# Kernel tuning notes

Hardware: AMD Instinct MI355X
Metric: run time of the kernel (lower is better)

## Reference

```python
import jax, jax.numpy as jnp
import numpy as np

N = 100_000   # nodes
E = 800_000   # edges
D = 128       # hidden_dim
L = 4         # layer_num
G = 512       # graphs in batch
T = 10        # target_dim
BN_EPS = 1e-5


def setup_inputs() -> dict:
    key = jax.random.key(0)
    ks = jax.random.split(key, 16)
    return {
        "x": jax.random.randint(ks[0], (N, 9), 0, 64),
        "edge_index": jax.random.randint(ks[1], (2, E), 0, N),
        "batch": jnp.sort(jax.random.randint(ks[2], (N,), 0, G)),
        "edge_attr": jax.random.randint(ks[3], (E, 3), 0, 8),
        "atom_emb": jax.random.normal(ks[4], (9, 64, D), jnp.float32) * 0.1,
        "W": jax.random.normal(ks[5], (L, D, D), jnp.float32) * 0.05,
        "b": jax.random.normal(ks[6], (L, D), jnp.float32) * 0.01,
        "root": jax.random.normal(ks[7], (L, D), jnp.float32) * 0.1,
        "bond_emb": jax.random.normal(ks[8], (L, 3, 8, D), jnp.float32) * 0.1,
        "gamma": jnp.ones((L, D), jnp.float32),
        "beta": jnp.zeros((L, D), jnp.float32),
        "W1": jax.random.normal(ks[9], (D, D), jnp.float32) * 0.05,
        "b1": jax.random.normal(ks[10], (D,), jnp.float32) * 0.01,
        "W2": jax.random.normal(ks[11], (D, T), jnp.float32) * 0.05,
        "b2": jax.random.normal(ks[12], (T,), jnp.float32) * 0.01,
    }


def reference(x, edge_index, batch, edge_attr, atom_emb, W, b, root,
              bond_emb, gamma, beta, W1, b1, W2, b2):
    # AtomEncoder: sum of 9 per-feature embeddings -> [N, D]
    h = atom_emb[jnp.arange(9)[None, :], x].sum(axis=1)

    row, col = edge_index[0], edge_index[1]  # source j, target i
    # degree(row, N) + 1 (same every layer)
    deg = jax.ops.segment_sum(jnp.ones((E,), h.dtype), row, num_segments=N) + 1.0
    dinv = deg ** -0.5
    norm = dinv[row] * dinv[col]  # [E]

    feat3 = jnp.arange(3)[None, :]
    for l in range(L):
        hl = h @ W[l] + b[l]                                   # linear
        e = bond_emb[l][feat3, edge_attr].sum(axis=1)          # BondEncoder [E, D]
        msg = norm[:, None] * jax.nn.relu(hl[row] + e)         # gather + message
        aggr = jax.ops.segment_sum(msg, col, num_segments=N)   # scatter-add
        h = aggr + jax.nn.relu(hl + root[l]) / deg[:, None]
        if l < L - 1:
            mu = h.mean(axis=0)
            var = jnp.var(h, axis=0)                           # biased, as torch BN train
            h = (h - mu) / jnp.sqrt(var + BN_EPS) * gamma[l] + beta[l]
            h = jax.nn.relu(h)
        # dropout is identity in eval mode

    # global mean pool over graphs
    counts = jax.ops.segment_sum(jnp.ones((N,), h.dtype), batch, num_segments=G)
    hg = jax.ops.segment_sum(h, batch, num_segments=G) / jnp.maximum(counts, 1.0)[:, None]

    # output MLP: ReLU -> Linear -> ReLU -> Linear
    hh = jax.nn.relu(hg)
    hh = jax.nn.relu(hh @ W1 + b1)
    return hh @ W2 + b2
```

## Files before the change

### kernel.cpp

```cpp
#include <hip/hip_runtime.h>
#include <hip/hip_fp16.h>

#define NN 100000
#define NE 800000
#define DD 128
#define NL 4
#define NG 512
#define NT 10
#define BN_EPS 1e-5f
#define SCAN_B 1024
#define CHUNK 7

typedef __attribute__((ext_vector_type(4))) float f32x4;
typedef __attribute__((ext_vector_type(8))) _Float16 f16x8;

__device__ __forceinline__ float atomAddF(float* p, float v) {
  return unsafeAtomicAdd(p, v);
}


__global__ __launch_bounds__(256) void edge_count_kernel(
    const int* __restrict__ ei, int* __restrict__ degcnt,
    int* __restrict__ incnt, int* __restrict__ erank) {
  int t = blockIdx.x * 256 + threadIdx.x;
  if (t * 4 >= NE) return;
  int4 s = *reinterpret_cast<const int4*>(&ei[t * 4]);
  int4 d = *reinterpret_cast<const int4*>(&ei[NE + t * 4]);
  atomicAdd(&degcnt[s.x], 1);
  atomicAdd(&degcnt[s.y], 1);
  atomicAdd(&degcnt[s.z], 1);
  atomicAdd(&degcnt[s.w], 1);
  int4 r;
  r.x = atomicAdd(&incnt[d.x], 1);
  r.y = atomicAdd(&incnt[d.y], 1);
  r.z = atomicAdd(&incnt[d.z], 1);
  r.w = atomicAdd(&incnt[d.w], 1);
  *reinterpret_cast<int4*>(&erank[t * 4]) = r;
}


__global__ __launch_bounds__(256) void tables_kernel(
    const float* __restrict__ W, __half* __restrict__ Wf,
    const float* __restrict__ atom_emb, __half* __restrict__ aemb16,
    const int* __restrict__ batch, int* __restrict__ gstart) {
  const int idx = blockIdx.x * 256 + threadIdx.x;
  if (idx < NL * 8 * 4 * 64) {
    int lane = idx & 63;
    int c = (idx >> 6) & 3;
    int t = (idx >> 8) & 7;
    int l = idx >> 11;
    const float* Wl = W + l * DD * DD;
    __half* o = Wf + idx * 8;
    int n = t * 16 + (lane & 15);
    int k0 = c * 32 + (lane >> 4) * 8;
#pragma unroll
    for (int i = 0; i < 8; ++i) o[i] = (__half)Wl[(k0 + i) * DD + n];
  }
  if (idx < 9 * 64 * 32) {
    float4 v = *reinterpret_cast<const float4*>(&atom_emb[idx * 4]);
    union { __half2 hh[2]; int2 i2; } u;
    u.hh[0] = __floats2half2_rn(v.x, v.y);
    u.hh[1] = __floats2half2_rn(v.z, v.w);
    *reinterpret_cast<int2*>(&aemb16[idx * 4]) = u.i2;
  }
  if (idx <= NG) {
    if (idx == NG) {
      gstart[NG] = NN;
    } else {
      int lo = 0, hi = NN;
      while (lo < hi) {
        int m = (lo + hi) >> 1;
        if (batch[m] < idx) lo = m + 1; else hi = m;
      }
      gstart[idx] = lo;
    }
  }
}


__global__ __launch_bounds__(256) void atom_encoder_kernel(
    const int* __restrict__ x, const __half* __restrict__ aemb16,
    __half* __restrict__ h) {
  __shared__ int xs[16 * 9];
  const int nb = blockIdx.x * 16;
  const int t = threadIdx.x;
  if (t < 144) {
    int gi = nb * 9 + t;
    xs[t] = (gi < NN * 9) ? x[gi] : 0;
  }
  __syncthreads();
  const int n = nb + (t >> 4);
  const int q8 = t & 15;
  if (n >= NN) return;
  const f16x8* av = reinterpret_cast<const f16x8*>(aemb16);
  float acc[8] = {};
#pragma unroll
  for (int f = 0; f < 9; ++f) {
    int r = xs[(t >> 4) * 9 + f];
    f16x8 v = av[(f * 64 + r) * 16 + q8];
#pragma unroll
    for (int i = 0; i < 8; ++i) acc[i] += (float)v[i];
  }
  union { __half2 hh[4]; int4 i4; } u;
#pragma unroll
  for (int i = 0; i < 4; ++i)
    u.hh[i] = __floats2half2_rn(acc[2 * i], acc[2 * i + 1]);
  *reinterpret_cast<int4*>(&h[n * DD + q8 * 8]) = u.i4;
}


__global__ __launch_bounds__(256) void scan1_kernel(
    const int* __restrict__ in, int* __restrict__ out, int* __restrict__ bsum,
    const int* __restrict__ degcnt, float* __restrict__ degrecip,
    float* __restrict__ dinv, int n) {
  __shared__ int s[256];
  int base = blockIdx.x * SCAN_B + threadIdx.x * 4;
  int v[4] = {0, 0, 0, 0};
  if (base + 3 < n) {
    int4 t = *reinterpret_cast<const int4*>(&in[base]);
    v[0] = t.x; v[1] = t.y; v[2] = t.z; v[3] = t.w;
  } else {
    for (int i = 0; i < 4; ++i) v[i] = (base + i < n) ? in[base + i] : 0;
  }
  for (int i = 0; i < 4; ++i) {
    if (base + i < n) {
      float dv = (float)degcnt[base + i] + 1.f;
      degrecip[base + i] = 1.f / dv;
      dinv[base + i] = rsqrtf(dv);
    }
  }
  int tsum = v[0] + v[1] + v[2] + v[3];
  s[threadIdx.x] = tsum;
  __syncthreads();
  for (int d = 1; d < 256; d <<= 1) {
    int t = (threadIdx.x >= d) ? s[threadIdx.x - d] : 0;
    __syncthreads();
    s[threadIdx.x] += t;
    __syncthreads();
  }
  int run = s[threadIdx.x] - tsum;
  if (threadIdx.x == 255) bsum[blockIdx.x] = s[255];
  for (int i = 0; i < 4; ++i) {
    if (base + i < n) out[base + i] = run;
    run += v[i];
  }
}

__global__ void scan2_kernel(int* bsum, int nb) {
  __shared__ int s[128];
  int v = (threadIdx.x < nb) ? bsum[threadIdx.x] : 0;
  s[threadIdx.x] = v;
  __syncthreads();
  for (int d = 1; d < 128; d <<= 1) {
    int t = (threadIdx.x >= d) ? s[threadIdx.x - d] : 0;
    __syncthreads();
    s[threadIdx.x] += t;
    __syncthreads();
  }
  if (threadIdx.x < nb) bsum[threadIdx.x] = s[threadIdx.x] - v;
}

__global__ __launch_bounds__(256) void scan3_kernel(int* off, const int* bsum,
                                                    int n, int total) {
  int i = blockIdx.x * 256 + threadIdx.x;
  if (i < n) off[i] += bsum[i / SCAN_B];
  if (i == 0) off[n] = total;
}

__global__ __launch_bounds__(256) void csr_fill_kernel(
    const int* __restrict__ ei, const int* __restrict__ eattr,
    const float* __restrict__ dinv, const int* __restrict__ off,
    const int* __restrict__ erank, int2* __restrict__ edata) {
  int e = blockIdx.x * 256 + threadIdx.x;
  if (e >= NE) return;
  int r = ei[e], c = ei[NE + e];
  int pos = off[c] + erank[e];
  float nm = dinv[r] * dinv[c];
  int idx9 = eattr[e * 3] | (eattr[e * 3 + 1] << 3) | (eattr[e * 3 + 2] << 6);
  int2 d;
  d.x = r | (idx9 << 17);
  d.y = __float_as_int(nm);
  edata[pos] = d;
}


__global__ __launch_bounds__(256) void gemm_mfma_kernel(
    const __half* __restrict__ A, const __half* __restrict__ Wf,
    const float* __restrict__ bias, const float* __restrict__ bn_scale,
    const float* __restrict__ bn_shift, int fuse_bn, __half* __restrict__ hl) {
  const int wid = threadIdx.x >> 6, lane = threadIdx.x & 63;
  const int r0 = blockIdx.x * 64 + wid * 16;
  const int arow = min(r0 + (lane & 15), NN - 1);
  const int kb = (lane >> 4) * 8;

  f16x8 afrag[4];
#pragma unroll
  for (int c = 0; c < 4; ++c) {
    const int k0 = c * 32 + kb;
    f16x8 raw = *reinterpret_cast<const f16x8*>(&A[arow * DD + k0]);
    if (fuse_bn) {
#pragma unroll
      for (int i = 0; i < 8; ++i) {
        float v = fmaxf((float)raw[i] * bn_scale[k0 + i] + bn_shift[k0 + i], 0.f);
        raw[i] = (_Float16)v;
      }
    }
    afrag[c] = raw;
  }

  f32x4 acc[8];
#pragma unroll
  for (int t = 0; t < 8; ++t) acc[t] = (f32x4){0.f, 0.f, 0.f, 0.f};

  const f16x8* __restrict__ wf = reinterpret_cast<const f16x8*>(Wf);
#pragma unroll
  for (int t = 0; t < 8; ++t) {
#pragma unroll
    for (int c = 0; c < 4; ++c) {
      f16x8 b = wf[(t * 4 + c) * 64 + lane];
      acc[t] = __builtin_amdgcn_mfma_f32_16x16x32_f16(afrag[c], b, acc[t], 0, 0, 0);
    }
  }

  const int colb = lane & 15;
  const int rbase = r0 + (lane >> 4) * 4;
#pragma unroll
  for (int t = 0; t < 8; ++t) {
    float bb = bias[t * 16 + colb];
#pragma unroll
    for (int j = 0; j < 4; ++j) {
      int row = rbase + j;
      if (row < NN) hl[row * DD + t * 16 + colb] = (__half)(acc[t][j] + bb);
    }
  }
}


#define PROC(E)                                                       \
  {                                                                   \
    int p_ = (E).x;                                                   \
    float nm_ = __int_as_float((E).y);                                \
    float2 hv_ = __half22float2(hl2[(p_ & 0x1FFFF) * 64 + lane]);     \
    int i9_ = p_ >> 17;                                               \
    float2 b0_ = __half22float2(bembS[(i9_ & 7) * 64 + lane]);        \
    float2 b1_ = __half22float2(bembS[(8 + ((i9_ >> 3) & 7)) * 64 + lane]); \
    float2 b2_ = __half22float2(bembS[(16 + ((i9_ >> 6) & 7)) * 64 + lane]); \
    acc0 += nm_ * fmaxf(hv_.x + b0_.x + b1_.x + b2_.x, 0.f);          \
    acc1 += nm_ * fmaxf(hv_.y + b0_.y + b1_.y + b2_.y, 0.f);          \
  }

__global__ __launch_bounds__(256) void gather_update_kernel(
    const int* __restrict__ off, const int2* __restrict__ edata,
    const __half2* __restrict__ hl2, const float* __restrict__ bemb,
    const float* __restrict__ root, const float* __restrict__ degrecip,
    const int* __restrict__ batch, __half2* __restrict__ h2,
    float* __restrict__ hg, float* __restrict__ bn_sum,
    float* __restrict__ bn_sq, int mode) {
  __shared__ __half2 bembS[24 * 64];
  const float2* bemb2 = reinterpret_cast<const float2*>(bemb);
  for (int i = threadIdx.x; i < 24 * 64; i += 256) {
    float2 v = bemb2[i];
    bembS[i] = __floats2half2_rn(v.x, v.y);
  }
  const int wid = threadIdx.x >> 6;
  const int lane = threadIdx.x & 63;
  float2 rt = *reinterpret_cast<const float2*>(&root[2 * lane]);
  float ls0 = 0, ls1 = 0, lq0 = 0, lq1 = 0;
  const int wv = blockIdx.x * 4 + wid;
  const int n0 = wv * CHUNK;
  const int n1 = min(n0 + CHUNK, NN);
  int curg = -1;
  float pg0 = 0.f, pg1 = 0.f;
  __syncthreads();
  for (int n = n0; n < n1; ++n) {
    int k0 = off[n], k1 = off[n + 1];
    float acc0 = 0.f, acc1 = 0.f;
    int k = k0;
    for (; k + 3 < k1; k += 4) {
      int2 e0 = edata[k], e1 = edata[k + 1], e2 = edata[k + 2],
           e3 = edata[k + 3];
      PROC(e0) PROC(e1) PROC(e2) PROC(e3)
    }
    for (; k < k1; ++k) {
      int2 e0 = edata[k];
      PROC(e0)
    }
    float dr = degrecip[n];
    float2 hs = __half22float2(hl2[n * 64 + lane]);
    float v0 = acc0 + fmaxf(hs.x + rt.x, 0.f) * dr;
    float v1 = acc1 + fmaxf(hs.y + rt.y, 0.f) * dr;
    if (mode == 0) {
      h2[n * 64 + lane] = __floats2half2_rn(v0, v1);
      ls0 += v0; ls1 += v1;
      lq0 += v0 * v0; lq1 += v1 * v1;
    } else {
      int g = batch[n];
      if (g != curg) {
        if (curg >= 0) {
          atomAddF(&hg[curg * DD + 2 * lane], pg0);
          atomAddF(&hg[curg * DD + 2 * lane + 1], pg1);
        }
        curg = g;
        pg0 = v0; pg1 = v1;
      } else {
        pg0 += v0; pg1 += v1;
      }
    }
  }
  if (mode == 1) {
    if (curg >= 0) {
      atomAddF(&hg[curg * DD + 2 * lane], pg0);
      atomAddF(&hg[curg * DD + 2 * lane + 1], pg1);
    }
    return;
  }
  __shared__ float s0[DD], s1[DD];
  const int d0 = 2 * lane, d1 = 2 * lane + 1;
  if (wid == 0) {
    s0[d0] = ls0; s0[d1] = ls1;
    s1[d0] = lq0; s1[d1] = lq1;
  }
  __syncthreads();
#pragma unroll
  for (int w = 1; w < 4; ++w) {
    if (wid == w) {
      s0[d0] += ls0; s0[d1] += ls1;
      s1[d0] += lq0; s1[d1] += lq1;
    }
    __syncthreads();
  }
  if (threadIdx.x < DD) {
    atomAddF(&bn_sum[threadIdx.x], s0[threadIdx.x]);
    atomAddF(&bn_sq[threadIdx.x], s1[threadIdx.x]);
  }
}

__global__ __launch_bounds__(128) void bn_finalize_kernel(
    const float* __restrict__ bn_sum, const float* __restrict__ bn_sq,
    const float* __restrict__ gamma, const float* __restrict__ beta,
    float* __restrict__ scale, float* __restrict__ shift) {
  int d = threadIdx.x;
  float mu = bn_sum[d] / (float)NN;
  float var = bn_sq[d] / (float)NN - mu * mu;
  float inv = rsqrtf(var + BN_EPS);
  float sc = gamma[d] * inv;
  scale[d] = sc;
  shift[d] = beta[d] - mu * sc;
}


__global__ __launch_bounds__(128) void mlp_kernel(
    const float* __restrict__ hg, const int* __restrict__ gstart,
    const float* __restrict__ W1, const float* __restrict__ b1,
    const float* __restrict__ W2, const float* __restrict__ b2,
    float* __restrict__ out) {
  int g = blockIdx.x, t = threadIdx.x;
  float cnt = fmaxf((float)(gstart[g + 1] - gstart[g]), 1.f);
  __shared__ float row[DD], t1[DD];
  row[t] = fmaxf(hg[g * DD + t] / cnt, 0.f);
  __syncthreads();
  float a1v = b1[t];
  for (int k = 0; k < DD; ++k) a1v = fmaf(row[k], W1[k * DD + t], a1v);
  t1[t] = fmaxf(a1v, 0.f);
  __syncthreads();
  if (t < NT) {
    float a2 = b2[t];
    for (int k = 0; k < DD; ++k) a2 = fmaf(t1[k], W2[k * NT + t], a2);
    out[g * NT + t] = a2;
  }
}

extern "C" void kernel_launch(void* const* d_in, const int* in_sizes, int n_in,
                              void* d_out, int out_size, void* d_ws,
                              size_t ws_size, hipStream_t stream) {
  const int* x = (const int*)d_in[0];
  const int* edge_index = (const int*)d_in[1];
  const int* batch = (const int*)d_in[2];
  const int* edge_attr = (const int*)d_in[3];
  const float* atom_emb = (const float*)d_in[4];
  const float* W = (const float*)d_in[5];
  const float* b = (const float*)d_in[6];
  const float* root = (const float*)d_in[7];
  const float* bond_emb = (const float*)d_in[8];
  const float* gamma = (const float*)d_in[9];
  const float* beta = (const float*)d_in[10];
  const float* W1 = (const float*)d_in[11];
  const float* b1 = (const float*)d_in[12];
  const float* W2 = (const float*)d_in[13];
  const float* b2 = (const float*)d_in[14];
  float* out = (float*)d_out;

  char* ws = (char*)d_ws;
  size_t off_b = 0;
  auto alloc = [&](size_t bytes) {
    char* p = ws + off_b;
    off_b += (bytes + 255) & ~size_t(255);
    return p;
  };
  __half* h = (__half*)alloc(sizeof(__half) * NN * DD);
  __half* hl = (__half*)alloc(sizeof(__half) * NN * DD);
  int2* edata = (int2*)alloc(sizeof(int2) * NE);
  int* erank = (int*)alloc(sizeof(int) * NE);
  float* degrecip = (float*)alloc(sizeof(float) * NN);
  float* dinv = (float*)alloc(sizeof(float) * NN);
  int* off = (int*)alloc(sizeof(int) * (NN + 1));
  int* bsum = (int*)alloc(sizeof(int) * 128);
  float* bsc = (float*)alloc(sizeof(float) * DD);
  float* bsh = (float*)alloc(sizeof(float) * DD);
  int* gstart = (int*)alloc(sizeof(int) * (NG + 1));
  __half* Wf = (__half*)alloc(sizeof(__half) * NL * DD * DD);
  __half* aemb16 = (__half*)alloc(sizeof(__half) * 9 * 64 * DD);
  char* zstart = ws + off_b;
  int* degcnt = (int*)alloc(sizeof(int) * NN);
  int* incnt = (int*)alloc(sizeof(int) * NN);
  float* hg = (float*)alloc(sizeof(float) * NG * DD);
  float* bnS = (float*)alloc(sizeof(float) * NL * DD);
  float* bnQ = (float*)alloc(sizeof(float) * NL * DD);
  size_t zbytes = (ws + off_b) - zstart;

  hipMemsetAsync(zstart, 0, zbytes, stream);

  edge_count_kernel<<<(NE / 4 + 255) / 256, 256, 0, stream>>>(
      edge_index, degcnt, incnt, erank);
  tables_kernel<<<(9 * 64 * 32 + 255) / 256, 256, 0, stream>>>(
      W, Wf, atom_emb, aemb16, batch, gstart);
  atom_encoder_kernel<<<(NN * 16 + 255) / 256, 256, 0, stream>>>(x, aemb16, h);

  const int nb = (NN + SCAN_B - 1) / SCAN_B;
  scan1_kernel<<<nb, 256, 0, stream>>>(incnt, off, bsum, degcnt, degrecip,
                                       dinv, NN);
  scan2_kernel<<<1, 128, 0, stream>>>(bsum, nb);
  scan3_kernel<<<(NN + 255) / 256, 256, 0, stream>>>(off, bsum, NN, NE);
  csr_fill_kernel<<<(NE + 255) / 256, 256, 0, stream>>>(edge_index, edge_attr,
                                                        dinv, off, erank, edata);

  const int GB = (NN + 4 * CHUNK - 1) / (4 * CHUNK);
  for (int l = 0; l < NL; ++l) {
    gemm_mfma_kernel<<<(NN + 63) / 64, 256, 0, stream>>>(
        h, Wf + l * DD * DD, b + l * DD, bsc, bsh, l > 0 ? 1 : 0, hl);
    int mode = (l < NL - 1) ? 0 : 1;
    gather_update_kernel<<<GB, 256, 0, stream>>>(
        off, edata, (const __half2*)hl, bond_emb + l * 3 * 8 * DD,
        root + l * DD, degrecip, batch, (__half2*)h, hg, bnS + l * DD,
        bnQ + l * DD, mode);
    if (mode == 0) {
      bn_finalize_kernel<<<1, DD, 0, stream>>>(bnS + l * DD, bnQ + l * DD,
                                               gamma + l * DD, beta + l * DD,
                                               bsc, bsh);
    }
  }

  mlp_kernel<<<NG, DD, 0, stream>>>(hg, gstart, W1, b1, W2, b2, out);
}
```

Baseline: 666.1 us.

## Process each node with a half-wavefront using 4 features per lane

The gather kernel now gives each destination node to 32 lanes instead of a full 64-lane wavefront, so every lane loads 4 half-precision features (8 bytes) per edge. Two nodes share a wavefront and the edge loop runs to the larger of their two degrees, with a zeroed norm masking the extra edges. Bond embeddings stay fp32 in shared memory, and the BatchNorm partial sums are reduced with shared-memory atomics instead of serialized per-wave steps. This aims for wider loads and more nodes in flight per block, at the cost of divergence when the paired nodes have different degrees and more shared-memory traffic.

```diff
diff --git a/kernel.cpp b/kernel.cpp
--- a/kernel.cpp
+++ b/kernel.cpp
@@ -236,19 +236,6 @@
 }
 
 
-#define PROC(E)                                                       \
-  {                                                                   \
-    int p_ = (E).x;                                                   \
-    float nm_ = __int_as_float((E).y);                                \
-    float2 hv_ = __half22float2(hl2[(p_ & 0x1FFFF) * 64 + lane]);     \
-    int i9_ = p_ >> 17;                                               \
-    float2 b0_ = __half22float2(bembS[(i9_ & 7) * 64 + lane]);        \
-    float2 b1_ = __half22float2(bembS[(8 + ((i9_ >> 3) & 7)) * 64 + lane]); \
-    float2 b2_ = __half22float2(bembS[(16 + ((i9_ >> 6) & 7)) * 64 + lane]); \
-    acc0 += nm_ * fmaxf(hv_.x + b0_.x + b1_.x + b2_.x, 0.f);          \
-    acc1 += nm_ * fmaxf(hv_.y + b0_.y + b1_.y + b2_.y, 0.f);          \
-  }
-
 __global__ __launch_bounds__(256) void gather_update_kernel(
     const int* __restrict__ off, const int2* __restrict__ edata,
     const __half2* __restrict__ hl2, const float* __restrict__ bemb,
@@ -256,79 +243,100 @@
     const int* __restrict__ batch, __half2* __restrict__ h2,
     float* __restrict__ hg, float* __restrict__ bn_sum,
     float* __restrict__ bn_sq, int mode) {
-  __shared__ __half2 bembS[24 * 64];
+  __shared__ float2 bembS[24 * 64];
+  __shared__ float s0[DD], s1[DD];
   const float2* bemb2 = reinterpret_cast<const float2*>(bemb);
-  for (int i = threadIdx.x; i < 24 * 64; i += 256) {
-    float2 v = bemb2[i];
-    bembS[i] = __floats2half2_rn(v.x, v.y);
-  }
-  const int wid = threadIdx.x >> 6;
-  const int lane = threadIdx.x & 63;
-  float2 rt = *reinterpret_cast<const float2*>(&root[2 * lane]);
-  float ls0 = 0, ls1 = 0, lq0 = 0, lq1 = 0;
-  const int wv = blockIdx.x * 4 + wid;
+  for (int i = threadIdx.x; i < 24 * 64; i += 256) bembS[i] = bemb2[i];
+  if (mode == 0 && threadIdx.x < DD) {
+    s0[threadIdx.x] = 0.f;
+    s1[threadIdx.x] = 0.f;
+  }
+  const int sid = threadIdx.x >> 5;
+  const int sl = threadIdx.x & 31;
+  const int p0 = 2 * sl;
+  float4 rt = *reinterpret_cast<const float4*>(&root[4 * sl]);
+  float ls[4] = {0, 0, 0, 0}, lq[4] = {0, 0, 0, 0};
+  const int wv = blockIdx.x * 8 + sid;
   const int n0 = wv * CHUNK;
   const int n1 = min(n0 + CHUNK, NN);
   int curg = -1;
-  float pg0 = 0.f, pg1 = 0.f;
+  float pg[4] = {0, 0, 0, 0};
   __syncthreads();
   for (int n = n0; n < n1; ++n) {
     int k0 = off[n], k1 = off[n + 1];
-    float acc0 = 0.f, acc1 = 0.f;
-    int k = k0;
-    for (; k + 3 < k1; k += 4) {
-      int2 e0 = edata[k], e1 = edata[k + 1], e2 = edata[k + 2],
-           e3 = edata[k + 3];
-      PROC(e0) PROC(e1) PROC(e2) PROC(e3)
-    }
-    for (; k < k1; ++k) {
-      int2 e0 = edata[k];
-      PROC(e0)
+    int cnt = k1 - k0;
+    int mx = max(cnt, __shfl_xor(cnt, 32));
+    float a0 = 0.f, a1 = 0.f, a2 = 0.f, a3 = 0.f;
+    for (int i = 0; i < mx; i += 4) {
+      int2 e[4];
+#pragma unroll
+      for (int j = 0; j < 4; ++j) e[j] = edata[min(k0 + i + j, NE - 1)];
+      int2 hv[4];
+#pragma unroll
+      for (int j = 0; j < 4; ++j)
+        hv[j] = *reinterpret_cast<const int2*>(&hl2[(e[j].x & 0x1FFFF) * 64 + p0]);
+#pragma unroll
+      for (int j = 0; j < 4; ++j) {
+        float nm = ((i + j) < cnt) ? __int_as_float(e[j].y) : 0.f;
+        int i9 = e[j].x >> 17;
+        float2 h01 = __half22float2(*reinterpret_cast<__half2*>(&hv[j].x));
+        float2 h23 = __half22float2(*reinterpret_cast<__half2*>(&hv[j].y));
+        const float2* t0 = &bembS[(i9 & 7) * 64];
+        const float2* t1 = &bembS[(8 + ((i9 >> 3) & 7)) * 64];
+        const float2* t2 = &bembS[(16 + ((i9 >> 6) & 7)) * 64];
+        float2 b0a = t0[p0], b0b = t0[p0 + 1];
+        float2 b1a = t1[p0], b1b = t1[p0 + 1];
+        float2 b2a = t2[p0], b2b = t2[p0 + 1];
+        a0 += nm * fmaxf(h01.x + b0a.x + b1a.x + b2a.x, 0.f);
+        a1 += nm * fmaxf(h01.y + b0a.y + b1a.y + b2a.y, 0.f);
+        a2 += nm * fmaxf(h23.x + b0b.x + b1b.x + b2b.x, 0.f);
+        a3 += nm * fmaxf(h23.y + b0b.y + b1b.y + b2b.y, 0.f);
+      }
     }
     float dr = degrecip[n];
-    float2 hs = __half22float2(hl2[n * 64 + lane]);
-    float v0 = acc0 + fmaxf(hs.x + rt.x, 0.f) * dr;
-    float v1 = acc1 + fmaxf(hs.y + rt.y, 0.f) * dr;
+    int2 hs2 = *reinterpret_cast<const int2*>(&hl2[n * 64 + p0]);
+    float2 hs01 = __half22float2(*reinterpret_cast<__half2*>(&hs2.x));
+    float2 hs23 = __half22float2(*reinterpret_cast<__half2*>(&hs2.y));
+    float v0 = a0 + fmaxf(hs01.x + rt.x, 0.f) * dr;
+    float v1 = a1 + fmaxf(hs01.y + rt.y, 0.f) * dr;
+    float v2 = a2 + fmaxf(hs23.x + rt.z, 0.f) * dr;
+    float v3 = a3 + fmaxf(hs23.y + rt.w, 0.f) * dr;
     if (mode == 0) {
-      h2[n * 64 + lane] = __floats2half2_rn(v0, v1);
-      ls0 += v0; ls1 += v1;
-      lq0 += v0 * v0; lq1 += v1 * v1;
+      int2 o;
+      *reinterpret_cast<__half2*>(&o.x) = __floats2half2_rn(v0, v1);
+      *reinterpret_cast<__half2*>(&o.y) = __floats2half2_rn(v2, v3);
+      *reinterpret_cast<int2*>(&h2[n * 64 + p0]) = o;
+      ls[0] += v0; ls[1] += v1; ls[2] += v2; ls[3] += v3;
+      lq[0] += v0 * v0; lq[1] += v1 * v1; lq[2] += v2 * v2; lq[3] += v3 * v3;
     } else {
       int g = batch[n];
       if (g != curg) {
         if (curg >= 0) {
-          atomAddF(&hg[curg * DD + 2 * lane], pg0);
-          atomAddF(&hg[curg * DD + 2 * lane + 1], pg1);
+#pragma unroll
+          for (int j = 0; j < 4; ++j)
+            atomAddF(&hg[curg * DD + 4 * sl + j], pg[j]);
         }
         curg = g;
-        pg0 = v0; pg1 = v1;
+        pg[0] = v0; pg[1] = v1; pg[2] = v2; pg[3] = v3;
       } else {
-        pg0 += v0; pg1 += v1;
+        pg[0] += v0; pg[1] += v1; pg[2] += v2; pg[3] += v3;
       }
     }
   }
   if (mode == 1) {
     if (curg >= 0) {
-      atomAddF(&hg[curg * DD + 2 * lane], pg0);
-      atomAddF(&hg[curg * DD + 2 * lane + 1], pg1);
+#pragma unroll
+      for (int j = 0; j < 4; ++j)
+        atomAddF(&hg[curg * DD + 4 * sl + j], pg[j]);
     }
     return;
   }
-  __shared__ float s0[DD], s1[DD];
-  const int d0 = 2 * lane, d1 = 2 * lane + 1;
-  if (wid == 0) {
-    s0[d0] = ls0; s0[d1] = ls1;
-    s1[d0] = lq0; s1[d1] = lq1;
-  }
-  __syncthreads();
-#pragma unroll
-  for (int w = 1; w < 4; ++w) {
-    if (wid == w) {
-      s0[d0] += ls0; s0[d1] += ls1;
-      s1[d0] += lq0; s1[d1] += lq1;
-    }
-    __syncthreads();
-  }
+#pragma unroll
+  for (int j = 0; j < 4; ++j) {
+    atomicAdd(&s0[4 * sl + j], ls[j]);
+    atomicAdd(&s1[4 * sl + j], lq[j]);
+  }
+  __syncthreads();
   if (threadIdx.x < DD) {
     atomAddF(&bn_sum[threadIdx.x], s0[threadIdx.x]);
     atomAddF(&bn_sq[threadIdx.x], s1[threadIdx.x]);
@@ -434,7 +442,7 @@
   csr_fill_kernel<<<(NE + 255) / 256, 256, 0, stream>>>(edge_index, edge_attr,
                                                         dinv, off, erank, edata);
 
-  const int GB = (NN + 4 * CHUNK - 1) / (4 * CHUNK);
+  const int GB = (NN + 8 * CHUNK - 1) / (8 * CHUNK);
   for (int l = 0; l < NL; ++l) {
     gemm_mfma_kernel<<<(NN + 63) / 64, 256, 0, stream>>>(
         h, Wf + l * DD * DD, b + l * DD, bsc, bsh, l > 0 ? 1 : 0, hl);
```

Result: faster. 574.6 us (-13.7%).
